# Kernel optimization log

Hardware: AMD Instinct MI355X
Metric: run time of the kernel (lower is better)

The kernel has to match this reference:

```python
import jax, jax.numpy as jnp
import numpy as np

GAMMA = 2.0
EPS = 1e-12  # tf.nn.l2_normalize epsilon


def setup_inputs() -> dict:
    key = jax.random.key(0)
    k1, k2 = jax.random.split(key)
    B, H, W_, C = 8, 56, 56, 256
    x = jax.random.normal(k1, (B, H, W_, C), dtype=jnp.float32)
    W = jax.random.normal(k2, (C, C), dtype=jnp.float32) * 0.05
    return {"x": x, "W": W}


def reference(x, W):
    B, H, Wd, C = x.shape
    hw = H * Wd
    # transform branch: 1x1 conv, no bias (num_layers=1)
    t = jnp.einsum('bhwc,cd->bhwd', x, W).reshape(B, hw, C)
    # pixel affinity: cosine similarity (tf: -cosine_similarity == cos sim)
    xf = x.reshape(B, hw, C)
    inv_norm = jax.lax.rsqrt(jnp.maximum(jnp.sum(xf * xf, axis=-1, keepdims=True), EPS))
    xn = xf * inv_norm
    sim = jnp.einsum('bic,bjc->bij', xn, xn)  # [B, hw, hw]
    sim = jnp.power(jax.nn.relu(sim), GAMMA)
    y = jnp.einsum('bij,bjc->bic', sim, t)
    return y.reshape(B, H, Wd, C)
```

## Files before the change

kernel.cpp:

```cpp
#include <hip/hip_runtime.h>

#define HW 3136
#define CH 256
#define NJT 49
#define NIT 25
#define NPIX 25088

typedef __attribute__((ext_vector_type(8))) short bf16x8;
typedef __attribute__((ext_vector_type(4))) float f32x4;
typedef __attribute__((ext_vector_type(16))) float f32x16;
typedef unsigned short u16;
typedef unsigned int u32;

static __device__ __forceinline__ u16 f2bf(float f){
  union { float f; u32 u; } v; v.f = f;
  u32 r = v.u + 0x7FFFu + ((v.u >> 16) & 1u);
  return (u16)(r >> 16);
}

static __device__ __forceinline__ void gload16(const void* g, void* l){
  __builtin_amdgcn_global_load_lds(
      (const __attribute__((address_space(1))) unsigned int*)g,
      (__attribute__((address_space(3))) unsigned int*)l, 16, 0, 0);
}

static __device__ __forceinline__ f32x16 zero16(){
  f32x16 v;
  #pragma unroll
  for (int e = 0; e < 16; ++e) v[e] = 0.f;
  return v;
}

#define MFMA32(A,B,C) __builtin_amdgcn_mfma_f32_32x32x16_bf16((A),(B),(C),0,0,0)

__global__ __launch_bounds__(256) void prep_wt(const float* __restrict__ W,
                                               u16* __restrict__ Wt){
  const int o = blockIdx.x, i = threadIdx.x;
  Wt[o*CH + i] = f2bf(W[i*CH + o]);
}

__global__ __launch_bounds__(256) void gemm_t(const float* __restrict__ x,
                                              const u16* __restrict__ Wt,
                                              u16* __restrict__ xn_bf,
                                              u16* __restrict__ tT){
  __shared__ u16 sT[256*64];
  const int jt = blockIdx.x, b = blockIdx.y;
  const int tid = threadIdx.x, wid = tid >> 6, lane = tid & 63;
  const int l15 = lane & 15, l4 = lane >> 4;
  const int j0 = jt * 64;
  const int row = j0 + wid*16 + l15;
  const float* xp = x + ((size_t)b*HW + row)*CH + l4*8;

  float xv[8][8];
  float ss = 0.f;
  #pragma unroll
  for (int kb = 0; kb < 8; ++kb){
    const float4 v0 = *(const float4*)(xp + kb*32);
    const float4 v1 = *(const float4*)(xp + kb*32 + 4);
    xv[kb][0]=v0.x; xv[kb][1]=v0.y; xv[kb][2]=v0.z; xv[kb][3]=v0.w;
    xv[kb][4]=v1.x; xv[kb][5]=v1.y; xv[kb][6]=v1.z; xv[kb][7]=v1.w;
    #pragma unroll
    for (int e = 0; e < 8; ++e) ss += xv[kb][e]*xv[kb][e];
  }
  ss += __shfl_xor(ss, 16);
  ss += __shfl_xor(ss, 32);
  const float inv = rsqrtf(fmaxf(ss, 1e-12f));

  bf16x8 ax[8];
  #pragma unroll
  for (int kb = 0; kb < 8; ++kb){
    bf16x8 a, n;
    #pragma unroll
    for (int e = 0; e < 8; ++e){
      a[e] = (short)f2bf(xv[kb][e]);
      n[e] = (short)f2bf(xv[kb][e]*inv);
    }
    ax[kb] = a;
    *(bf16x8*)(xn_bf + ((size_t)b*HW + row)*CH + kb*32 + l4*8) = n;
  }

  f32x4 acc[16];
  #pragma unroll
  for (int n = 0; n < 16; ++n) acc[n] = f32x4{0.f,0.f,0.f,0.f};
  #pragma unroll
  for (int kb = 0; kb < 8; ++kb){
    #pragma unroll
    for (int n0 = 0; n0 < 16; ++n0){
      const bf16x8 bb = *(const bf16x8*)(Wt + (n0*16 + l15)*CH + kb*32 + l4*8);
      acc[n0] = __builtin_amdgcn_mfma_f32_16x16x32_bf16(ax[kb], bb, acc[n0], 0, 0, 0);
    }
  }
  #pragma unroll
  for (int n0 = 0; n0 < 16; ++n0){
    const int c = n0*16 + l15;
    const int jloc = wid*16 + l4*4;
    const int gj = jloc >> 3;
    ushort4 w4;
    w4.x = f2bf(acc[n0][0]); w4.y = f2bf(acc[n0][1]);
    w4.z = f2bf(acc[n0][2]); w4.w = f2bf(acc[n0][3]);
    *(ushort4*)&sT[c*64 + ((gj ^ (c & 7)) * 8) + (jloc & 7)] = w4;
  }
  __syncthreads();
  #pragma unroll
  for (int p = 0; p < 8; ++p){
    const int c = p*32 + (tid >> 3);
    const int q = tid & 7;
    const bf16x8 v = *(const bf16x8*)&sT[c*64 + ((q ^ (c & 7)) * 8)];
    *(bf16x8*)(tT + ((size_t)b*CH + c)*HW + j0 + q*8) = v;
  }
}

__global__ __launch_bounds__(512) void ppm_main(const u16* __restrict__ xn,
                                                const u16* __restrict__ tT,
                                                float* __restrict__ out){
  __shared__ u16 SM[81920];

  const int it = blockIdx.x, b = blockIdx.y;
  const int tid = threadIdx.x, wid = tid >> 6, lane = tid & 63;
  const int l31 = lane & 31, hi = lane >> 5;
  const int i0 = it * 128;
  const int wj = wid >> 2, wi = wid & 3;

  bf16x8 aq[16];
  {
    int irow = i0 + wi*32 + l31;
    if (irow >= HW) irow = HW - 1;
    const u16* p = xn + ((size_t)b*HW + irow)*CH + hi*8;
    #pragma unroll
    for (int ks = 0; ks < 16; ++ks) aq[ks] = *(const bf16x8*)(p + ks*16);
  }

  f32x16 accY[4];
  #pragma unroll
  for (int cb = 0; cb < 4; ++cb) accY[cb] = zero16();

  const size_t xbase = (size_t)b*HW;
  const size_t tbase = (size_t)b*CH;

  auto STAGE_XN = [&](int jt){
    u16* dst = SM + (jt & 1)*16384;
    const int j0n = jt*64;
    #pragma unroll
    for (int q = 0; q < 4; ++q){
      const int m = q*512 + tid;
      const int row = m >> 5, g = m & 31;
      gload16(xn + (xbase + j0n + row)*CH + ((g ^ (row & 7))*8), &dst[m*8]);
    }
  };
  auto STAGE_TT = [&](int jt){
    u16* dst = SM + 32768 + (jt & 1)*16384;
    const int j0n = jt*64;
    #pragma unroll
    for (int q = 0; q < 4; ++q){
      const int m = q*512 + tid;
      const int c = m >> 3, g = m & 7;
      gload16(tT + (tbase + c)*HW + j0n + ((g ^ (c & 7))*8), &dst[m*8]);
    }
  };

  auto PV = [&](int p){
    const u16* sTJp = SM + 32768 + (p & 1)*16384;
    const u16* sPBp = SM + 65536 + (p & 1)*8192;
    bf16x8 pb[4];
    #pragma unroll
    for (int ks = 0; ks < 4; ++ks)
      pb[ks] = *(const bf16x8*)&sPBp[(wi*4 + ks)*512 + lane*8];
    __builtin_amdgcn_s_setprio(1);
    #pragma unroll
    for (int ks = 0; ks < 4; ++ks){
      #pragma unroll
      for (int cb = 0; cb < 4; ++cb){
        const int c = wj*128 + cb*32 + l31;
        const bf16x8 af = *(const bf16x8*)&sTJp[c*64 + (((ks*2 + hi) ^ (c & 7)) * 8)];
        accY[cb] = MFMA32(af, pb[ks], accY[cb]);
      }
    }
    __builtin_amdgcn_s_setprio(0);
  };

  STAGE_XN(0);
  __syncthreads();

  #pragma unroll 1
  for (int jt = 0; jt < NJT; ++jt){
    if (jt + 1 < NJT) STAGE_XN(jt + 1);
    STAGE_TT(jt);

    if (jt > 0) PV(jt - 1);

    const u16* sXJk = SM + (jt & 1)*16384;
    f32x16 sa = zero16(), sb = zero16();
    const int rj = wj*32 + l31;
    const int rsw = rj & 7;
    const u16* xjrow = &sXJk[rj*256];
    __builtin_amdgcn_s_setprio(1);
    #pragma unroll
    for (int kb = 0; kb < 8; ++kb){
      const bf16x8 a0 = *(const bf16x8*)&xjrow[(((kb*4 + hi)     ^ rsw) * 8)];
      const bf16x8 a1 = *(const bf16x8*)&xjrow[(((kb*4 + 2 + hi) ^ rsw) * 8)];
      sa = MFMA32(a0, aq[2*kb],   sa);
      sb = MFMA32(a1, aq[2*kb+1], sb);
    }
    __builtin_amdgcn_s_setprio(0);

    float s0,s1,s2,s3,s4,s5,s6,s7,s8,s9,s10,s11,s12,s13,s14,s15;
#define SREL(d, r) { float v_ = sa[r] + sb[r]; v_ = fmaxf(v_, 0.f); d = v_ * v_; }
    SREL(s0,0) SREL(s1,1) SREL(s2,2) SREL(s3,3) SREL(s4,4) SREL(s5,5) SREL(s6,6) SREL(s7,7)
    SREL(s8,8) SREL(s9,9) SREL(s10,10) SREL(s11,11) SREL(s12,12) SREL(s13,13) SREL(s14,14) SREL(s15,15)
#undef SREL
    u32 w0,w1,w2,w3,w4,w5,w6,w7;
#define PK(d, a, c) asm("v_cvt_pk_bf16_f32 %0, %1, %2" : "=v"(d) : "v"(a), "v"(c));
    PK(w0, s0, s1)  PK(w1, s2, s3)  PK(w2, s4, s5)  PK(w3, s6, s7)
    PK(w4, s8, s9)  PK(w5, s10,s11) PK(w6, s12,s13) PK(w7, s14,s15)
#undef PK
    asm volatile("v_permlane32_swap_b32 %0, %1" : "+v"(w0), "+v"(w2));
    asm volatile("v_permlane32_swap_b32 %0, %1" : "+v"(w1), "+v"(w3));
    asm volatile("v_permlane32_swap_b32 %0, %1" : "+v"(w4), "+v"(w6));
    asm volatile("v_permlane32_swap_b32 %0, %1" : "+v"(w5), "+v"(w7));
    union { u32 u[4]; bf16x8 v; } fb0, fb1;
    fb0.u[0]=w0; fb0.u[1]=w1; fb0.u[2]=w2; fb0.u[3]=w3;
    fb1.u[0]=w4; fb1.u[1]=w5; fb1.u[2]=w6; fb1.u[3]=w7;

    u16* sPBk = SM + 65536 + (jt & 1)*8192;
    *(bf16x8*)&sPBk[(wi*4 + 2*wj + 0)*512 + lane*8] = fb0.v;
    *(bf16x8*)&sPBk[(wi*4 + 2*wj + 1)*512 + lane*8] = fb1.v;

    __syncthreads();
  }

  PV(NJT - 1);
  __syncthreads();

  float* Yl = (float*)SM;
  {
    const int il = wi*32 + l31;
    const int isw = (il & 7) << 2;
    #pragma unroll
    for (int cb = 0; cb < 4; ++cb)
      #pragma unroll
      for (int r = 0; r < 16; ++r){
        const int c = wj*128 + cb*32 + (r & 3) + 8*(r >> 2) + 4*hi;
        Yl[il*256 + (c ^ isw)] = accY[cb][r];
      }
  }
  __syncthreads();
  {
    const int i3 = tid >> 2;
    const int cq = (tid & 3) * 64;
    const int sw3 = (i3 & 7) << 2;
    if (i0 + i3 < HW){
      float* orow = out + ((size_t)b*HW + i0 + i3)*CH;
      #pragma unroll
      for (int q = 0; q < 16; ++q){
        const int c = cq + q*4;
        const float4 v = *(const float4*)&Yl[i3*256 + (c ^ sw3)];
        *(float4*)&orow[c] = v;
      }
    }
  }
}

extern "C" void kernel_launch(void* const* d_in, const int* in_sizes, int n_in,
                              void* d_out, int out_size, void* d_ws, size_t ws_size,
                              hipStream_t stream){
  const float* x = (const float*)d_in[0];
  const float* W = (const float*)d_in[1];
  float* out = (float*)d_out;
  char* ws = (char*)d_ws;

  const size_t SZ = (size_t)NPIX * CH * sizeof(u16);
  u16* xn_bf = (u16*)(ws);
  u16* tT    = (u16*)(ws + SZ);
  u16* Wt    = (u16*)(ws + 2*SZ);

  prep_wt<<<CH, CH, 0, stream>>>(W, Wt);
  gemm_t<<<dim3(NJT, 8), 256, 0, stream>>>(x, Wt, xn_bf, tT);
  ppm_main<<<dim3(NIT, 8), 512, 0, stream>>>(xn_bf, tT, out);
}
```

Baseline: 150.3 us.

## Retile PV warps to 64x64 blocks, widen LDS swizzle, remap block order

Result: no change. 153.1 us (+1.9%).

```diff
diff --git a/kernel.cpp b/kernel.cpp
--- a/kernel.cpp
+++ b/kernel.cpp
@@ -115,11 +115,16 @@
                                                 float* __restrict__ out){
   __shared__ u16 SM[81920];
 
-  const int it = blockIdx.x, b = blockIdx.y;
+  const int bid = blockIdx.x;
+  const int swz = (bid & 7)*25 + (bid >> 3);
+  const int b = swz / 25;
+  const int it = swz % 25;
+
   const int tid = threadIdx.x, wid = tid >> 6, lane = tid & 63;
   const int l31 = lane & 31, hi = lane >> 5;
   const int i0 = it * 128;
   const int wj = wid >> 2, wi = wid & 3;
+  const int ih = wi >> 1, cq = wj*2 + (wi & 1);
 
   bf16x8 aq[16];
   {
@@ -130,9 +135,11 @@
     for (int ks = 0; ks < 16; ++ks) aq[ks] = *(const bf16x8*)(p + ks*16);
   }
 
-  f32x16 accY[4];
-  #pragma unroll
-  for (int cb = 0; cb < 4; ++cb) accY[cb] = zero16();
+  f32x16 accY[2][2];
+  #pragma unroll
+  for (int cb = 0; cb < 2; ++cb)
+    #pragma unroll
+    for (int ibx = 0; ibx < 2; ++ibx) accY[cb][ibx] = zero16();
 
   const size_t xbase = (size_t)b*HW;
   const size_t tbase = (size_t)b*CH;
@@ -144,7 +151,7 @@
     for (int q = 0; q < 4; ++q){
       const int m = q*512 + tid;
       const int row = m >> 5, g = m & 31;
-      gload16(xn + (xbase + j0n + row)*CH + ((g ^ (row & 7))*8), &dst[m*8]);
+      gload16(xn + (xbase + j0n + row)*CH + ((g ^ (row & 15))*8), &dst[m*8]);
     }
   };
   auto STAGE_TT = [&](int jt){
@@ -161,18 +168,22 @@
   auto PV = [&](int p){
     const u16* sTJp = SM + 32768 + (p & 1)*16384;
     const u16* sPBp = SM + 65536 + (p & 1)*8192;
-    bf16x8 pb[4];
+    bf16x8 pb[4][2];
     #pragma unroll
     for (int ks = 0; ks < 4; ++ks)
-      pb[ks] = *(const bf16x8*)&sPBp[(wi*4 + ks)*512 + lane*8];
+      #pragma unroll
+      for (int ibx = 0; ibx < 2; ++ibx)
+        pb[ks][ibx] = *(const bf16x8*)&sPBp[((ih*2 + ibx)*4 + ks)*512 + lane*8];
     __builtin_amdgcn_s_setprio(1);
     #pragma unroll
     for (int ks = 0; ks < 4; ++ks){
       #pragma unroll
-      for (int cb = 0; cb < 4; ++cb){
-        const int c = wj*128 + cb*32 + l31;
+      for (int cb = 0; cb < 2; ++cb){
+        const int c = cq*64 + cb*32 + l31;
         const bf16x8 af = *(const bf16x8*)&sTJp[c*64 + (((ks*2 + hi) ^ (c & 7)) * 8)];
-        accY[cb] = MFMA32(af, pb[ks], accY[cb]);
+        #pragma unroll
+        for (int ibx = 0; ibx < 2; ++ibx)
+          accY[cb][ibx] = MFMA32(af, pb[ks][ibx], accY[cb][ibx]);
       }
     }
     __builtin_amdgcn_s_setprio(0);
@@ -191,7 +202,7 @@
     const u16* sXJk = SM + (jt & 1)*16384;
     f32x16 sa = zero16(), sb = zero16();
     const int rj = wj*32 + l31;
-    const int rsw = rj & 7;
+    const int rsw = rj & 15;
     const u16* xjrow = &sXJk[rj*256];
     __builtin_amdgcn_s_setprio(1);
     #pragma unroll
@@ -233,26 +244,29 @@
 
   float* Yl = (float*)SM;
   {
-    const int il = wi*32 + l31;
-    const int isw = (il & 7) << 2;
-    #pragma unroll
-    for (int cb = 0; cb < 4; ++cb)
-      #pragma unroll
-      for (int r = 0; r < 16; ++r){
-        const int c = wj*128 + cb*32 + (r & 3) + 8*(r >> 2) + 4*hi;
-        Yl[il*256 + (c ^ isw)] = accY[cb][r];
+    #pragma unroll
+    for (int cb = 0; cb < 2; ++cb)
+      #pragma unroll
+      for (int ibx = 0; ibx < 2; ++ibx){
+        const int il = ih*64 + ibx*32 + l31;
+        const int isw = (il & 7) << 2;
+        #pragma unroll
+        for (int r = 0; r < 16; ++r){
+          const int c = cq*64 + cb*32 + (r & 3) + 8*(r >> 2) + 4*hi;
+          Yl[il*256 + (c ^ isw)] = accY[cb][ibx][r];
+        }
       }
   }
   __syncthreads();
   {
     const int i3 = tid >> 2;
-    const int cq = (tid & 3) * 64;
+    const int cq4 = (tid & 3) * 64;
     const int sw3 = (i3 & 7) << 2;
     if (i0 + i3 < HW){
       float* orow = out + ((size_t)b*HW + i0 + i3)*CH;
       #pragma unroll
       for (int q = 0; q < 16; ++q){
-        const int c = cq + q*4;
+        const int c = cq4 + q*4;
         const float4 v = *(const float4*)&Yl[i3*256 + (c ^ sw3)];
         *(float4*)&orow[c] = v;
       }
@@ -275,5 +289,5 @@
 
   prep_wt<<<CH, CH, 0, stream>>>(W, Wt);
   gemm_t<<<dim3(NJT, 8), 256, 0, stream>>>(x, Wt, xn_bf, tT);
-  ppm_main<<<dim3(NIT, 8), 512, 0, stream>>>(xn_bf, tT, out);
-}
+  ppm_main<<<200, 512, 0, stream>>>(xn_bf, tT, out);
+}
```

## Halve ppm_main tile to 64 rows, single-buffer LDS, swizzle grid across XCDs

Applied to the files above, without the earlier changes.

After: 236.7 us. +57.5%, slower.

```diff
diff --git a/kernel.cpp b/kernel.cpp
--- a/kernel.cpp
+++ b/kernel.cpp
@@ -3,7 +3,6 @@
 #define HW 3136
 #define CH 256
 #define NJT 49
-#define NIT 25
 #define NPIX 25088
 
 typedef __attribute__((ext_vector_type(8))) short bf16x8;
@@ -110,22 +109,25 @@
   }
 }
 
-__global__ __launch_bounds__(512) void ppm_main(const u16* __restrict__ xn,
+__global__ __launch_bounds__(256) void ppm_main(const u16* __restrict__ xn,
                                                 const u16* __restrict__ tT,
                                                 float* __restrict__ out){
-  __shared__ u16 SM[81920];
-
-  const int it = blockIdx.x, b = blockIdx.y;
+  __shared__ u16 SM[40960];
+
+  const int bid = blockIdx.x;
+  const int swz = (bid & 7)*49 + (bid >> 3);
+  const int b = swz / 49;
+  const int it = swz % 49;
+
   const int tid = threadIdx.x, wid = tid >> 6, lane = tid & 63;
   const int l31 = lane & 31, hi = lane >> 5;
-  const int i0 = it * 128;
-  const int wj = wid >> 2, wi = wid & 3;
+  const int i0 = it * 64;
+  const int wj = wid >> 1, wi = wid & 1;
+  const int ih = wid >> 1, ch = wid & 1;
 
   bf16x8 aq[16];
   {
-    int irow = i0 + wi*32 + l31;
-    if (irow >= HW) irow = HW - 1;
-    const u16* p = xn + ((size_t)b*HW + irow)*CH + hi*8;
+    const u16* p = xn + ((size_t)b*HW + i0 + wi*32 + l31)*CH + hi*8;
     #pragma unroll
     for (int ks = 0; ks < 16; ++ks) aq[ks] = *(const bf16x8*)(p + ks*16);
   }
@@ -138,39 +140,39 @@
   const size_t tbase = (size_t)b*CH;
 
   auto STAGE_XN = [&](int jt){
-    u16* dst = SM + (jt & 1)*16384;
+    u16* dst = SM;
     const int j0n = jt*64;
     #pragma unroll
-    for (int q = 0; q < 4; ++q){
-      const int m = q*512 + tid;
+    for (int q = 0; q < 8; ++q){
+      const int m = q*256 + tid;
       const int row = m >> 5, g = m & 31;
-      gload16(xn + (xbase + j0n + row)*CH + ((g ^ (row & 7))*8), &dst[m*8]);
+      gload16(xn + (xbase + j0n + row)*CH + ((g ^ (row & 15))*8), &dst[m*8]);
     }
   };
   auto STAGE_TT = [&](int jt){
-    u16* dst = SM + 32768 + (jt & 1)*16384;
+    u16* dst = SM + 16384;
     const int j0n = jt*64;
     #pragma unroll
-    for (int q = 0; q < 4; ++q){
-      const int m = q*512 + tid;
+    for (int q = 0; q < 8; ++q){
+      const int m = q*256 + tid;
       const int c = m >> 3, g = m & 7;
       gload16(tT + (tbase + c)*HW + j0n + ((g ^ (c & 7))*8), &dst[m*8]);
     }
   };
 
   auto PV = [&](int p){
-    const u16* sTJp = SM + 32768 + (p & 1)*16384;
-    const u16* sPBp = SM + 65536 + (p & 1)*8192;
+    const u16* sTJp = SM + 16384;
+    const u16* sPBp = SM + 32768 + (p & 1)*4096;
     bf16x8 pb[4];
     #pragma unroll
     for (int ks = 0; ks < 4; ++ks)
-      pb[ks] = *(const bf16x8*)&sPBp[(wi*4 + ks)*512 + lane*8];
+      pb[ks] = *(const bf16x8*)&sPBp[(ih*4 + ks)*512 + lane*8];
     __builtin_amdgcn_s_setprio(1);
     #pragma unroll
     for (int ks = 0; ks < 4; ++ks){
       #pragma unroll
       for (int cb = 0; cb < 4; ++cb){
-        const int c = wj*128 + cb*32 + l31;
+        const int c = ch*128 + cb*32 + l31;
         const bf16x8 af = *(const bf16x8*)&sTJp[c*64 + (((ks*2 + hi) ^ (c & 7)) * 8)];
         accY[cb] = MFMA32(af, pb[ks], accY[cb]);
       }
@@ -183,16 +185,12 @@
 
   #pragma unroll 1
   for (int jt = 0; jt < NJT; ++jt){
-    if (jt + 1 < NJT) STAGE_XN(jt + 1);
-    STAGE_TT(jt);
-
     if (jt > 0) PV(jt - 1);
 
-    const u16* sXJk = SM + (jt & 1)*16384;
     f32x16 sa = zero16(), sb = zero16();
     const int rj = wj*32 + l31;
-    const int rsw = rj & 7;
-    const u16* xjrow = &sXJk[rj*256];
+    const int rsw = rj & 15;
+    const u16* xjrow = &SM[rj*256];
     __builtin_amdgcn_s_setprio(1);
     #pragma unroll
     for (int kb = 0; kb < 8; ++kb){
@@ -221,11 +219,16 @@
     fb0.u[0]=w0; fb0.u[1]=w1; fb0.u[2]=w2; fb0.u[3]=w3;
     fb1.u[0]=w4; fb1.u[1]=w5; fb1.u[2]=w6; fb1.u[3]=w7;
 
-    u16* sPBk = SM + 65536 + (jt & 1)*8192;
+    u16* sPBk = SM + 32768 + (jt & 1)*4096;
     *(bf16x8*)&sPBk[(wi*4 + 2*wj + 0)*512 + lane*8] = fb0.v;
     *(bf16x8*)&sPBk[(wi*4 + 2*wj + 1)*512 + lane*8] = fb1.v;
 
     __syncthreads();
+
+    if (jt + 1 < NJT) STAGE_XN(jt + 1);
+    STAGE_TT(jt);
+
+    __syncthreads();
   }
 
   PV(NJT - 1);
@@ -233,29 +236,27 @@
 
   float* Yl = (float*)SM;
   {
-    const int il = wi*32 + l31;
+    const int il = ih*32 + l31;
     const int isw = (il & 7) << 2;
     #pragma unroll
     for (int cb = 0; cb < 4; ++cb)
       #pragma unroll
       for (int r = 0; r < 16; ++r){
-        const int c = wj*128 + cb*32 + (r & 3) + 8*(r >> 2) + 4*hi;
+        const int c = ch*128 + cb*32 + (r & 3) + 8*(r >> 2) + 4*hi;
         Yl[il*256 + (c ^ isw)] = accY[cb][r];
       }
   }
   __syncthreads();
   {
     const int i3 = tid >> 2;
-    const int cq = (tid & 3) * 64;
+    const int cq4 = (tid & 3) * 64;
     const int sw3 = (i3 & 7) << 2;
-    if (i0 + i3 < HW){
-      float* orow = out + ((size_t)b*HW + i0 + i3)*CH;
-      #pragma unroll
-      for (int q = 0; q < 16; ++q){
-        const int c = cq + q*4;
-        const float4 v = *(const float4*)&Yl[i3*256 + (c ^ sw3)];
-        *(float4*)&orow[c] = v;
-      }
+    float* orow = out + ((size_t)b*HW + i0 + i3)*CH;
+    #pragma unroll
+    for (int q = 0; q < 16; ++q){
+      const int c = cq4 + q*4;
+      const float4 v = *(const float4*)&Yl[i3*256 + (c ^ sw3)];
+      *(float4*)&orow[c] = v;
     }
   }
 }
@@ -275,5 +276,5 @@
 
   prep_wt<<<CH, CH, 0, stream>>>(W, Wt);
   gemm_t<<<dim3(NJT, 8), 256, 0, stream>>>(x, Wt, xn_bf, tT);
-  ppm_main<<<dim3(NIT, 8), 512, 0, stream>>>(xn_bf, tT, out);
-}
+  ppm_main<<<392, 256, 0, stream>>>(xn_bf, tT, out);
+}
```
